# Kernel optimization log

Hardware: AMD Instinct MI355X
Metric: run time of the kernel (lower is better)

The kernel has to match this reference:

```python
import jax, jax.numpy as jnp
import numpy as np

EPS = 1e-15
PROJ_EPS = 1e-5
N_NODES = 100000

def _norm(x):
    return jnp.maximum(jnp.sqrt(jnp.sum(x * x, axis=-1, keepdims=True)), EPS)

def _tanh(x):
    return jnp.tanh(jnp.clip(x, -15.0, 15.0))

def _atanh(x):
    return jnp.arctanh(jnp.clip(x, -1.0 + 1e-7, 1.0 - 1e-7))

def log_map_zero(y):
    n = _norm(y)
    return (_atanh(n) / n) * y

def exp_map_zero(v):
    n = _norm(v)
    return (_tanh(n) / n) * v

def hyperbolic_projection(x):
    # clip norm to 1 - PROJ_EPS (stay inside the Poincare ball)
    n = _norm(x)
    scale = jnp.minimum(jnp.float32(1.0), (1.0 - PROJ_EPS) / n)
    return x * scale

def mobius_addition(x, y):
    x2 = jnp.sum(x * x, axis=-1, keepdims=True)
    y2 = jnp.sum(y * y, axis=-1, keepdims=True)
    xy = jnp.sum(x * y, axis=-1, keepdims=True)
    num = (1.0 + 2.0 * xy + y2) * x + (1.0 - x2) * y
    den = 1.0 + 2.0 * xy + x2 * y2
    return num / jnp.maximum(den, EPS)

def setup_inputs() -> dict:
    key = jax.random.key(0)
    k0, k1, k2, k3, k4, k5 = jax.random.split(key, 6)
    N, E, D_IN, D_OUT = N_NODES, 640000, 128, 128
    # entity embeddings: points inside the Poincare ball
    x = jax.random.normal(k0, (N, D_IN), dtype=jnp.float32) * 0.01
    x = hyperbolic_projection(x)
    # xavier-uniform weight
    a = np.sqrt(6.0 / (D_IN + D_OUT)).astype(np.float32)
    W = jax.random.uniform(k1, (D_IN, D_OUT), minval=-a, maxval=a, dtype=jnp.float32)
    bias = jax.random.normal(k2, (1, D_OUT), dtype=jnp.float32) * 0.01
    adj_row = jax.random.randint(k3, (E,), 0, N, dtype=jnp.int32)
    adj_col = jax.random.randint(k4, (E,), 0, N, dtype=jnp.int32)
    adj_val = jax.random.uniform(k5, (E,), dtype=jnp.float32) * 0.125
    return {"ents_embed_input": x, "W_ent": W, "bias_vec": bias,
            "adj_val": adj_val, "adj_row": adj_row, "adj_col": adj_col}

def reference(ents_embed_input, W_ent, bias_vec, adj_val, adj_row, adj_col):
    # log map to tangent space at origin, then dense linear map
    tangent = log_map_zero(ents_embed_input)                 # [N, D_in]
    mapped = tangent @ W_ent                                 # [N, D_out]
    # sparse adjacency aggregation: out[i] = sum_e val[e] * mapped[col[e]], row[e] == i
    msgs = adj_val[:, None] * mapped[adj_col]                # [E, D_out]
    agg = jax.ops.segment_sum(msgs, adj_row, num_segments=N_NODES)
    h = hyperbolic_projection(exp_map_zero(agg))
    # mobius bias addition
    b = hyperbolic_projection(exp_map_zero(bias_vec))
    out = hyperbolic_projection(mobius_addition(h, b))
    return out
```

## Files before the change

### kernel.cpp

```cpp
#include <hip/hip_runtime.h>
#include <hip/hip_bf16.h>

#define D 128
#define FEPS 1e-15f
#define PROJ_EPS 1e-5f

typedef __attribute__((ext_vector_type(8))) short short8v;
typedef __attribute__((ext_vector_type(4))) float f32x4;

__device__ __forceinline__ unsigned pack_bf16x2(float lo, float hi) {
    __hip_bfloat16 h0 = __float2bfloat16(lo);
    __hip_bfloat16 h1 = __float2bfloat16(hi);
    unsigned u0 = *reinterpret_cast<unsigned short*>(&h0);
    unsigned u1 = *reinterpret_cast<unsigned short*>(&h1);
    return u0 | (u1 << 16);
}

__device__ __forceinline__ float bf_lo(unsigned u) { return __uint_as_float(u << 16); }
__device__ __forceinline__ float bf_hi(unsigned u) { return __uint_as_float(u & 0xffff0000u); }

__device__ __forceinline__ float fast_tanh_clamped(float n) {
    float nc = fminf(n, 15.f);
    float e2 = __expf(2.f * nc);
    return 1.f - __fdividef(2.f, e2 + 1.f);
}

__global__ __launch_bounds__(512) void k_gemm_hist(
    const float* __restrict__ x, const float* __restrict__ W,
    __hip_bfloat16* __restrict__ mapped, int Nn,
    const int* __restrict__ rowi, int* __restrict__ cnt, int E, int GB, int HB)
{
    __shared__ uint4 ls4[2048];

    const int tid = threadIdx.x;

    if (blockIdx.x >= GB) {
        int stride = HB * 512;
        for (int e = (blockIdx.x - GB) * 512 + tid; e < E; e += stride)
            atomicAdd(&cnt[rowi[e]], 1);
        return;
    }

    const int w = tid >> 6, l = tid & 63;
    const int q = l & 15, khi = l >> 4;

#pragma unroll
    for (int it = 0; it < 4; ++it) {
        int i = it * 512 + tid;
        int col = i & 127, kg = i >> 7;
        unsigned p0 = pack_bf16x2(W[(kg * 8 + 0) * D + col], W[(kg * 8 + 1) * D + col]);
        unsigned p1 = pack_bf16x2(W[(kg * 8 + 2) * D + col], W[(kg * 8 + 3) * D + col]);
        unsigned p2 = pack_bf16x2(W[(kg * 8 + 4) * D + col], W[(kg * 8 + 5) * D + col]);
        unsigned p3 = pack_bf16x2(W[(kg * 8 + 6) * D + col], W[(kg * 8 + 7) * D + col]);
        ls4[col * 16 + (kg ^ (col & 15))] = make_uint4(p0, p1, p2, p3);
    }

    const int rowbase = blockIdx.x * 128;
    const int row = rowbase + w * 16 + q;
    const bool rv = row < Nn;
    const float* xr = x + (size_t)row * D;
    float4 xa[8];
    float nn = 0.f;
#pragma unroll
    for (int ks = 0; ks < 4; ++ks) {
        float4 p0 = make_float4(0.f, 0.f, 0.f, 0.f), p1 = p0;
        if (rv) {
            p0 = *reinterpret_cast<const float4*>(xr + ks * 32 + khi * 8);
            p1 = *reinterpret_cast<const float4*>(xr + ks * 32 + khi * 8 + 4);
        }
        xa[2 * ks] = p0; xa[2 * ks + 1] = p1;
        nn += p0.x * p0.x + p0.y * p0.y + p0.z * p0.z + p0.w * p0.w
            + p1.x * p1.x + p1.y * p1.y + p1.z * p1.z + p1.w * p1.w;
    }
    nn += __shfl_xor(nn, 16, 64);
    nn += __shfl_xor(nn, 32, 64);
    float n = fmaxf(sqrtf(nn), FEPS);
    float c = fminf(n, 1.f - 1e-7f);
    float s = __fdividef(0.5f * __logf(__fdividef(1.f + c, 1.f - c)), n);

    union { unsigned u[4]; short8v v; } af[4];
#pragma unroll
    for (int ks = 0; ks < 4; ++ks) {
        float4 p0 = xa[2 * ks], p1 = xa[2 * ks + 1];
        af[ks].u[0] = pack_bf16x2(s * p0.x, s * p0.y);
        af[ks].u[1] = pack_bf16x2(s * p0.z, s * p0.w);
        af[ks].u[2] = pack_bf16x2(s * p1.x, s * p1.y);
        af[ks].u[3] = pack_bf16x2(s * p1.z, s * p1.w);
    }
    __syncthreads();

    f32x4 acc[8];
#pragma unroll
    for (int t = 0; t < 8; ++t) acc[t] = (f32x4){0.f, 0.f, 0.f, 0.f};

    const short8v* lsB = (const short8v*)ls4;
#pragma unroll
    for (int ks = 0; ks < 4; ++ks) {
#pragma unroll
        for (int t = 0; t < 8; ++t) {
            short8v b = lsB[(t * 16 + q) * 16 + ((ks * 4 + khi) ^ q)];
            acc[t] = __builtin_amdgcn_mfma_f32_16x16x32_bf16(af[ks].v, b, acc[t], 0, 0, 0);
        }
    }
    __syncthreads();

    unsigned* lsw = (unsigned*)ls4;
    const int rlbase = w * 16;
#pragma unroll
    for (int t = 0; t < 8; ++t) {
#pragma unroll
        for (int r = 0; r < 4; ++r) {
            float self = acc[t][r];
            float other = __shfl_xor(self, 1, 64);
            unsigned pw = (q & 1) ? pack_bf16x2(other, self) : pack_bf16x2(self, other);
            int rl = rlbase + khi * 4 + r;
            int cp = t * 8 + (q >> 1);
            lsw[rl * 64 + (cp ^ (khi << 3))] = pw;
        }
    }
#pragma unroll
    for (int i4 = 0; i4 < 4; ++i4) {
        int rl = rlbase + i4 * 4 + (l >> 4);
        int ro = rowbase + rl;
        int cp4 = (l & 15) * 4;
        uint4 vv = ls4[(rl * 64 + (cp4 ^ (((rl >> 2) & 3) << 3))) >> 2];
        if (ro < Nn)
            *reinterpret_cast<uint4*>(mapped + (size_t)ro * D + (l & 15) * 8) = vv;
    }
}

__global__ __launch_bounds__(256) void k_scan1(const int* __restrict__ cnt,
                                               int* __restrict__ ex,
                                               int* __restrict__ bsum, int Nn) {
    __shared__ int ts[256];
    int t = threadIdx.x, b = blockIdx.x;
    int base = b * 1024 + t * 4;
    int v0 = (base + 0 < Nn) ? cnt[base + 0] : 0;
    int v1 = (base + 1 < Nn) ? cnt[base + 1] : 0;
    int v2 = (base + 2 < Nn) ? cnt[base + 2] : 0;
    int v3 = (base + 3 < Nn) ? cnt[base + 3] : 0;
    int s = v0 + v1 + v2 + v3;
    ts[t] = s;
    __syncthreads();
    for (int off = 1; off < 256; off <<= 1) {
        int add = (t >= off) ? ts[t - off] : 0;
        __syncthreads();
        ts[t] += add;
        __syncthreads();
    }
    int excl = ts[t] - s;
    if (t == 255) bsum[b] = ts[t];
    if (base + 0 < Nn) ex[base + 0] = excl;
    if (base + 1 < Nn) ex[base + 1] = excl + v0;
    if (base + 2 < Nn) ex[base + 2] = excl + v0 + v1;
    if (base + 3 < Nn) ex[base + 3] = excl + v0 + v1 + v2;
}

__global__ void k_scan2(const int* __restrict__ bsum, int* __restrict__ bsumx, int nb) {
    __shared__ int ts[128];
    int t = threadIdx.x;
    int v = (t < nb) ? bsum[t] : 0;
    ts[t] = v;
    __syncthreads();
    for (int off = 1; off < 128; off <<= 1) {
        int add = (t >= off) ? ts[t - off] : 0;
        __syncthreads();
        ts[t] += add;
        __syncthreads();
    }
    bsumx[t] = ts[t] - v;
}

__global__ __launch_bounds__(256) void k_scan3(int* __restrict__ rowptr,
                                               const int* __restrict__ bsumx,
                                               int* __restrict__ cursor, int Nn, int E) {
    int i = blockIdx.x * 256 + threadIdx.x;
    if (i < Nn) {
        int v = rowptr[i] + bsumx[i >> 10];
        rowptr[i] = v;
        cursor[i] = v;
    }
    if (i == 0) rowptr[Nn] = E;
}

__global__ __launch_bounds__(512) void k_scatter(
    const int* __restrict__ rowi, const int* __restrict__ coli,
    const float* __restrict__ val, int* __restrict__ cursor,
    int2* __restrict__ sedge, int E) {
    int e = blockIdx.x * 512 + threadIdx.x;
    if (e >= E) return;
    int cv = coli[e];
    float vv = val[e];
    int p = atomicAdd(&cursor[rowi[e]], 1);
    sedge[p] = make_int2(cv, __float_as_int(vv));
}

__global__ __launch_bounds__(256) void k_aggfin(
    const uint4* __restrict__ mapped4, const int2* __restrict__ sedge,
    const int* __restrict__ rowptr, const float* __restrict__ bias,
    float* __restrict__ out, int Nn)
{
    const int tid = threadIdx.x;
    const int w = tid >> 6, l = tid & 63;
    const int g = l >> 4, q = l & 15;
    const int row = blockIdx.x * 16 + w * 4 + g;

    float4 rb0 = *reinterpret_cast<const float4*>(bias + q * 8);
    float4 rb1 = *reinterpret_cast<const float4*>(bias + q * 8 + 4);
    float bn2 = rb0.x * rb0.x + rb0.y * rb0.y + rb0.z * rb0.z + rb0.w * rb0.w
              + rb1.x * rb1.x + rb1.y * rb1.y + rb1.z * rb1.z + rb1.w * rb1.w;
#pragma unroll
    for (int o = 8; o > 0; o >>= 1) bn2 += __shfl_xor(bn2, o, 64);
    float bn = fmaxf(sqrtf(bn2), FEPS);
    float bt = fast_tanh_clamped(bn);
    float bs = __fdividef(bt, bn);
    float ben2 = bs * bs * bn2;
    float bpn = fmaxf(sqrtf(ben2), FEPS);
    float bps = fminf(1.f, __fdividef(1.f - PROJ_EPS, bpn));
    float bsc = bs * bps;
    float y2 = bps * bps * ben2;
    float bj[8] = { rb0.x * bsc, rb0.y * bsc, rb0.z * bsc, rb0.w * bsc,
                    rb1.x * bsc, rb1.y * bsc, rb1.z * bsc, rb1.w * bsc };

    if (row >= Nn) return;
    int beg = rowptr[row], end = rowptr[row + 1];

    float acc[8] = {0.f, 0.f, 0.f, 0.f, 0.f, 0.f, 0.f, 0.f};
    int e = beg;
    for (; e + 3 < end; e += 4) {
        int2 d0 = sedge[e], d1 = sedge[e + 1], d2 = sedge[e + 2], d3 = sedge[e + 3];
        uint4 u0 = mapped4[(size_t)d0.x * 16 + q];
        uint4 u1 = mapped4[(size_t)d1.x * 16 + q];
        uint4 u2 = mapped4[(size_t)d2.x * 16 + q];
        uint4 u3 = mapped4[(size_t)d3.x * 16 + q];
        float v0 = __int_as_float(d0.y), v1 = __int_as_float(d1.y);
        float v2 = __int_as_float(d2.y), v3 = __int_as_float(d3.y);
        acc[0] += v0 * bf_lo(u0.x); acc[1] += v0 * bf_hi(u0.x);
        acc[2] += v0 * bf_lo(u0.y); acc[3] += v0 * bf_hi(u0.y);
        acc[4] += v0 * bf_lo(u0.z); acc[5] += v0 * bf_hi(u0.z);
        acc[6] += v0 * bf_lo(u0.w); acc[7] += v0 * bf_hi(u0.w);
        acc[0] += v1 * bf_lo(u1.x); acc[1] += v1 * bf_hi(u1.x);
        acc[2] += v1 * bf_lo(u1.y); acc[3] += v1 * bf_hi(u1.y);
        acc[4] += v1 * bf_lo(u1.z); acc[5] += v1 * bf_hi(u1.z);
        acc[6] += v1 * bf_lo(u1.w); acc[7] += v1 * bf_hi(u1.w);
        acc[0] += v2 * bf_lo(u2.x); acc[1] += v2 * bf_hi(u2.x);
        acc[2] += v2 * bf_lo(u2.y); acc[3] += v2 * bf_hi(u2.y);
        acc[4] += v2 * bf_lo(u2.z); acc[5] += v2 * bf_hi(u2.z);
        acc[6] += v2 * bf_lo(u2.w); acc[7] += v2 * bf_hi(u2.w);
        acc[0] += v3 * bf_lo(u3.x); acc[1] += v3 * bf_hi(u3.x);
        acc[2] += v3 * bf_lo(u3.y); acc[3] += v3 * bf_hi(u3.y);
        acc[4] += v3 * bf_lo(u3.z); acc[5] += v3 * bf_hi(u3.z);
        acc[6] += v3 * bf_lo(u3.w); acc[7] += v3 * bf_hi(u3.w);
    }
    for (; e < end; ++e) {
        int2 d0 = sedge[e];
        uint4 u0 = mapped4[(size_t)d0.x * 16 + q];
        float v0 = __int_as_float(d0.y);
        acc[0] += v0 * bf_lo(u0.x); acc[1] += v0 * bf_hi(u0.x);
        acc[2] += v0 * bf_lo(u0.y); acc[3] += v0 * bf_hi(u0.y);
        acc[4] += v0 * bf_lo(u0.z); acc[5] += v0 * bf_hi(u0.z);
        acc[6] += v0 * bf_lo(u0.w); acc[7] += v0 * bf_hi(u0.w);
    }

    float n2 = 0.f, ab = 0.f;
#pragma unroll
    for (int j = 0; j < 8; ++j) { n2 += acc[j] * acc[j]; ab += acc[j] * bj[j]; }
#pragma unroll
    for (int o = 8; o > 0; o >>= 1) {
        n2 += __shfl_xor(n2, o, 64);
        ab += __shfl_xor(ab, o, 64);
    }

    float n = fmaxf(sqrtf(n2), FEPS);
    float t = fast_tanh_clamped(n);
    float s = __fdividef(t, n);
    float en2 = s * s * n2;
    float pn = fmaxf(sqrtf(en2), FEPS);
    float ps = fminf(1.f, __fdividef(1.f - PROJ_EPS, pn));
    float hs = s * ps;
    float x2 = ps * ps * en2;

    float xy = hs * ab;
    float cA = 1.f + 2.f * xy + y2;
    float cB = 1.f - x2;
    float den = fmaxf(1.f + 2.f * xy + x2 * y2, FEPS);
    float inv = __fdividef(1.f, den);
    float zn2 = inv * inv * (cA * cA * x2 + 2.f * cA * cB * xy + cB * cB * y2);
    float zn = fmaxf(sqrtf(zn2), FEPS);
    float zs = fminf(1.f, __fdividef(1.f - PROJ_EPS, zn));
    float f = inv * zs;
    float chs = cA * hs * f, cBf = cB * f;

    float4 o0 = make_float4(chs * acc[0] + cBf * bj[0], chs * acc[1] + cBf * bj[1],
                            chs * acc[2] + cBf * bj[2], chs * acc[3] + cBf * bj[3]);
    float4 o1 = make_float4(chs * acc[4] + cBf * bj[4], chs * acc[5] + cBf * bj[5],
                            chs * acc[6] + cBf * bj[6], chs * acc[7] + cBf * bj[7]);
    *reinterpret_cast<float4*>(out + (size_t)row * D + q * 8) = o0;
    *reinterpret_cast<float4*>(out + (size_t)row * D + q * 8 + 4) = o1;
}

extern "C" void kernel_launch(void* const* d_in, const int* in_sizes, int n_in,
                              void* d_out, int out_size, void* d_ws, size_t ws_size,
                              hipStream_t stream) {
    const float* x    = (const float*)d_in[0];
    const float* W    = (const float*)d_in[1];
    const float* bias = (const float*)d_in[2];
    const float* val  = (const float*)d_in[3];
    const int*   rowi = (const int*)d_in[4];
    const int*   coli = (const int*)d_in[5];
    const int N = in_sizes[0] / D;
    const int E = in_sizes[3];

    char* ws = (char*)d_ws;
    int*   cnt    = (int*)ws;
    int*   rowptr = (int*)(ws + 400000);
    int*   bsum   = (int*)(ws + 800512);
    int*   bsumx  = (int*)(ws + 801024);
    int*   cursor = (int*)(ws + 801536);
    int2*  sedge  = (int2*)(ws + 1201536);
    __hip_bfloat16* mapped = (__hip_bfloat16*)(ws + 1201536 + (size_t)E * 8);
    float* out = (float*)d_out;

    hipMemsetAsync(cnt, 0, (size_t)N * sizeof(int), stream);

    const int GB = (N + 127) / 128;
    const int HB = 128;
    k_gemm_hist<<<GB + HB, 512, 0, stream>>>(x, W, mapped, N, rowi, cnt, E, GB, HB);

    int nb = (N + 1023) / 1024;
    k_scan1<<<nb, 256, 0, stream>>>(cnt, rowptr, bsum, N);
    k_scan2<<<1, 128, 0, stream>>>(bsum, bsumx, nb);
    k_scan3<<<(N + 255) / 256, 256, 0, stream>>>(rowptr, bsumx, cursor, N, E);

    k_scatter<<<(E + 511) / 512, 512, 0, stream>>>(rowi, coli, val, cursor, sedge, E);
    k_aggfin<<<(N + 15) / 16, 256, 0, stream>>>((const uint4*)mapped, sedge, rowptr,
                                                bias, out, N);
}
```

Measured before the change: 134.1 us.

## Halve gemm block size, use nontemporal edge stores, widen per-lane aggregation width

The GEMM/histogram kernel moves to 256-thread blocks of 64 rows, and the x loads are issued before the W staging so they overlap. The scatter kernel writes packed edge records with nontemporal stores. The aggregation kernel now maps 8 lanes per row with 16 columns each, so a wave covers 8 rows and each lane issues two 16-byte gathers per edge. This aims for more memory-level parallelism per row and less cache pollution, at the cost of more registers per lane and more W staging per block.

```diff
diff --git a/kernel.cpp b/kernel.cpp
--- a/kernel.cpp
+++ b/kernel.cpp
@@ -25,7 +25,18 @@
     return 1.f - __fdividef(2.f, e2 + 1.f);
 }
 
-__global__ __launch_bounds__(512) void k_gemm_hist(
+__device__ __forceinline__ void accum16(float* acc, uint4 a, uint4 b, float v) {
+    acc[0]  += v * bf_lo(a.x); acc[1]  += v * bf_hi(a.x);
+    acc[2]  += v * bf_lo(a.y); acc[3]  += v * bf_hi(a.y);
+    acc[4]  += v * bf_lo(a.z); acc[5]  += v * bf_hi(a.z);
+    acc[6]  += v * bf_lo(a.w); acc[7]  += v * bf_hi(a.w);
+    acc[8]  += v * bf_lo(b.x); acc[9]  += v * bf_hi(b.x);
+    acc[10] += v * bf_lo(b.y); acc[11] += v * bf_hi(b.y);
+    acc[12] += v * bf_lo(b.z); acc[13] += v * bf_hi(b.z);
+    acc[14] += v * bf_lo(b.w); acc[15] += v * bf_hi(b.w);
+}
+
+__global__ __launch_bounds__(256) void k_gemm_hist(
     const float* __restrict__ x, const float* __restrict__ W,
     __hip_bfloat16* __restrict__ mapped, int Nn,
     const int* __restrict__ rowi, int* __restrict__ cnt, int E, int GB, int HB)
@@ -35,8 +46,8 @@
     const int tid = threadIdx.x;
 
     if (blockIdx.x >= GB) {
-        int stride = HB * 512;
-        for (int e = (blockIdx.x - GB) * 512 + tid; e < E; e += stride)
+        int stride = HB * 256;
+        for (int e = (blockIdx.x - GB) * 256 + tid; e < E; e += stride)
             atomicAdd(&cnt[rowi[e]], 1);
         return;
     }
@@ -44,23 +55,11 @@
     const int w = tid >> 6, l = tid & 63;
     const int q = l & 15, khi = l >> 4;
 
-#pragma unroll
-    for (int it = 0; it < 4; ++it) {
-        int i = it * 512 + tid;
-        int col = i & 127, kg = i >> 7;
-        unsigned p0 = pack_bf16x2(W[(kg * 8 + 0) * D + col], W[(kg * 8 + 1) * D + col]);
-        unsigned p1 = pack_bf16x2(W[(kg * 8 + 2) * D + col], W[(kg * 8 + 3) * D + col]);
-        unsigned p2 = pack_bf16x2(W[(kg * 8 + 4) * D + col], W[(kg * 8 + 5) * D + col]);
-        unsigned p3 = pack_bf16x2(W[(kg * 8 + 6) * D + col], W[(kg * 8 + 7) * D + col]);
-        ls4[col * 16 + (kg ^ (col & 15))] = make_uint4(p0, p1, p2, p3);
-    }
-
-    const int rowbase = blockIdx.x * 128;
+    const int rowbase = blockIdx.x * 64;
     const int row = rowbase + w * 16 + q;
     const bool rv = row < Nn;
     const float* xr = x + (size_t)row * D;
     float4 xa[8];
-    float nn = 0.f;
 #pragma unroll
     for (int ks = 0; ks < 4; ++ks) {
         float4 p0 = make_float4(0.f, 0.f, 0.f, 0.f), p1 = p0;
@@ -69,8 +68,24 @@
             p1 = *reinterpret_cast<const float4*>(xr + ks * 32 + khi * 8 + 4);
         }
         xa[2 * ks] = p0; xa[2 * ks + 1] = p1;
-        nn += p0.x * p0.x + p0.y * p0.y + p0.z * p0.z + p0.w * p0.w
-            + p1.x * p1.x + p1.y * p1.y + p1.z * p1.z + p1.w * p1.w;
+    }
+
+#pragma unroll
+    for (int it = 0; it < 8; ++it) {
+        int i = it * 256 + tid;
+        int col = i & 127, kg = i >> 7;
+        unsigned p0 = pack_bf16x2(W[(kg * 8 + 0) * D + col], W[(kg * 8 + 1) * D + col]);
+        unsigned p1 = pack_bf16x2(W[(kg * 8 + 2) * D + col], W[(kg * 8 + 3) * D + col]);
+        unsigned p2 = pack_bf16x2(W[(kg * 8 + 4) * D + col], W[(kg * 8 + 5) * D + col]);
+        unsigned p3 = pack_bf16x2(W[(kg * 8 + 6) * D + col], W[(kg * 8 + 7) * D + col]);
+        ls4[col * 16 + (kg ^ (col & 15))] = make_uint4(p0, p1, p2, p3);
+    }
+
+    float nn = 0.f;
+#pragma unroll
+    for (int j = 0; j < 8; ++j) {
+        float4 p = xa[j];
+        nn += p.x * p.x + p.y * p.y + p.z * p.z + p.w * p.w;
     }
     nn += __shfl_xor(nn, 16, 64);
     nn += __shfl_xor(nn, 32, 64);
@@ -186,13 +201,14 @@
 __global__ __launch_bounds__(512) void k_scatter(
     const int* __restrict__ rowi, const int* __restrict__ coli,
     const float* __restrict__ val, int* __restrict__ cursor,
-    int2* __restrict__ sedge, int E) {
+    long long* __restrict__ sedge, int E) {
     int e = blockIdx.x * 512 + threadIdx.x;
     if (e >= E) return;
     int cv = coli[e];
     float vv = val[e];
     int p = atomicAdd(&cursor[rowi[e]], 1);
-    sedge[p] = make_int2(cv, __float_as_int(vv));
+    long long pkt = ((long long)(unsigned)__float_as_int(vv) << 32) | (unsigned)cv;
+    __builtin_nontemporal_store(pkt, &sedge[p]);
 }
 
 __global__ __launch_bounds__(256) void k_aggfin(
@@ -202,15 +218,20 @@
 {
     const int tid = threadIdx.x;
     const int w = tid >> 6, l = tid & 63;
-    const int g = l >> 4, q = l & 15;
-    const int row = blockIdx.x * 16 + w * 4 + g;
-
-    float4 rb0 = *reinterpret_cast<const float4*>(bias + q * 8);
-    float4 rb1 = *reinterpret_cast<const float4*>(bias + q * 8 + 4);
-    float bn2 = rb0.x * rb0.x + rb0.y * rb0.y + rb0.z * rb0.z + rb0.w * rb0.w
-              + rb1.x * rb1.x + rb1.y * rb1.y + rb1.z * rb1.z + rb1.w * rb1.w;
-#pragma unroll
-    for (int o = 8; o > 0; o >>= 1) bn2 += __shfl_xor(bn2, o, 64);
+    const int g = l >> 3, q = l & 7;
+    const int row = blockIdx.x * 32 + w * 8 + g;
+
+    float bj[16];
+    float bn2 = 0.f;
+#pragma unroll
+    for (int j = 0; j < 4; ++j) {
+        float4 rb = *reinterpret_cast<const float4*>(bias + q * 16 + j * 4);
+        bj[4 * j + 0] = rb.x; bj[4 * j + 1] = rb.y;
+        bj[4 * j + 2] = rb.z; bj[4 * j + 3] = rb.w;
+        bn2 += rb.x * rb.x + rb.y * rb.y + rb.z * rb.z + rb.w * rb.w;
+    }
+#pragma unroll
+    for (int o = 4; o > 0; o >>= 1) bn2 += __shfl_xor(bn2, o, 64);
     float bn = fmaxf(sqrtf(bn2), FEPS);
     float bt = fast_tanh_clamped(bn);
     float bs = __fdividef(bt, bn);
@@ -219,54 +240,40 @@
     float bps = fminf(1.f, __fdividef(1.f - PROJ_EPS, bpn));
     float bsc = bs * bps;
     float y2 = bps * bps * ben2;
-    float bj[8] = { rb0.x * bsc, rb0.y * bsc, rb0.z * bsc, rb0.w * bsc,
-                    rb1.x * bsc, rb1.y * bsc, rb1.z * bsc, rb1.w * bsc };
+#pragma unroll
+    for (int j = 0; j < 16; ++j) bj[j] *= bsc;
 
     if (row >= Nn) return;
     int beg = rowptr[row], end = rowptr[row + 1];
 
-    float acc[8] = {0.f, 0.f, 0.f, 0.f, 0.f, 0.f, 0.f, 0.f};
+    const uint4* mp = mapped4 + 2 * q;
+    float acc[16];
+#pragma unroll
+    for (int j = 0; j < 16; ++j) acc[j] = 0.f;
+
     int e = beg;
     for (; e + 3 < end; e += 4) {
         int2 d0 = sedge[e], d1 = sedge[e + 1], d2 = sedge[e + 2], d3 = sedge[e + 3];
-        uint4 u0 = mapped4[(size_t)d0.x * 16 + q];
-        uint4 u1 = mapped4[(size_t)d1.x * 16 + q];
-        uint4 u2 = mapped4[(size_t)d2.x * 16 + q];
-        uint4 u3 = mapped4[(size_t)d3.x * 16 + q];
-        float v0 = __int_as_float(d0.y), v1 = __int_as_float(d1.y);
-        float v2 = __int_as_float(d2.y), v3 = __int_as_float(d3.y);
-        acc[0] += v0 * bf_lo(u0.x); acc[1] += v0 * bf_hi(u0.x);
-        acc[2] += v0 * bf_lo(u0.y); acc[3] += v0 * bf_hi(u0.y);
-        acc[4] += v0 * bf_lo(u0.z); acc[5] += v0 * bf_hi(u0.z);
-        acc[6] += v0 * bf_lo(u0.w); acc[7] += v0 * bf_hi(u0.w);
-        acc[0] += v1 * bf_lo(u1.x); acc[1] += v1 * bf_hi(u1.x);
-        acc[2] += v1 * bf_lo(u1.y); acc[3] += v1 * bf_hi(u1.y);
-        acc[4] += v1 * bf_lo(u1.z); acc[5] += v1 * bf_hi(u1.z);
-        acc[6] += v1 * bf_lo(u1.w); acc[7] += v1 * bf_hi(u1.w);
-        acc[0] += v2 * bf_lo(u2.x); acc[1] += v2 * bf_hi(u2.x);
-        acc[2] += v2 * bf_lo(u2.y); acc[3] += v2 * bf_hi(u2.y);
-        acc[4] += v2 * bf_lo(u2.z); acc[5] += v2 * bf_hi(u2.z);
-        acc[6] += v2 * bf_lo(u2.w); acc[7] += v2 * bf_hi(u2.w);
-        acc[0] += v3 * bf_lo(u3.x); acc[1] += v3 * bf_hi(u3.x);
-        acc[2] += v3 * bf_lo(u3.y); acc[3] += v3 * bf_hi(u3.y);
-        acc[4] += v3 * bf_lo(u3.z); acc[5] += v3 * bf_hi(u3.z);
-        acc[6] += v3 * bf_lo(u3.w); acc[7] += v3 * bf_hi(u3.w);
+        uint4 a0 = mp[(size_t)d0.x * 16], b0 = mp[(size_t)d0.x * 16 + 1];
+        uint4 a1 = mp[(size_t)d1.x * 16], b1 = mp[(size_t)d1.x * 16 + 1];
+        uint4 a2 = mp[(size_t)d2.x * 16], b2 = mp[(size_t)d2.x * 16 + 1];
+        uint4 a3 = mp[(size_t)d3.x * 16], b3 = mp[(size_t)d3.x * 16 + 1];
+        accum16(acc, a0, b0, __int_as_float(d0.y));
+        accum16(acc, a1, b1, __int_as_float(d1.y));
+        accum16(acc, a2, b2, __int_as_float(d2.y));
+        accum16(acc, a3, b3, __int_as_float(d3.y));
     }
     for (; e < end; ++e) {
-        int2 d0 = sedge[e];
-        uint4 u0 = mapped4[(size_t)d0.x * 16 + q];
-        float v0 = __int_as_float(d0.y);
-        acc[0] += v0 * bf_lo(u0.x); acc[1] += v0 * bf_hi(u0.x);
-        acc[2] += v0 * bf_lo(u0.y); acc[3] += v0 * bf_hi(u0.y);
-        acc[4] += v0 * bf_lo(u0.z); acc[5] += v0 * bf_hi(u0.z);
-        acc[6] += v0 * bf_lo(u0.w); acc[7] += v0 * bf_hi(u0.w);
+        int2 d = sedge[e];
+        uint4 a = mp[(size_t)d.x * 16], b = mp[(size_t)d.x * 16 + 1];
+        accum16(acc, a, b, __int_as_float(d.y));
     }
 
     float n2 = 0.f, ab = 0.f;
 #pragma unroll
-    for (int j = 0; j < 8; ++j) { n2 += acc[j] * acc[j]; ab += acc[j] * bj[j]; }
-#pragma unroll
-    for (int o = 8; o > 0; o >>= 1) {
+    for (int j = 0; j < 16; ++j) { n2 += acc[j] * acc[j]; ab += acc[j] * bj[j]; }
+#pragma unroll
+    for (int o = 4; o > 0; o >>= 1) {
         n2 += __shfl_xor(n2, o, 64);
         ab += __shfl_xor(ab, o, 64);
     }
@@ -291,12 +298,14 @@
     float f = inv * zs;
     float chs = cA * hs * f, cBf = cB * f;
 
-    float4 o0 = make_float4(chs * acc[0] + cBf * bj[0], chs * acc[1] + cBf * bj[1],
-                            chs * acc[2] + cBf * bj[2], chs * acc[3] + cBf * bj[3]);
-    float4 o1 = make_float4(chs * acc[4] + cBf * bj[4], chs * acc[5] + cBf * bj[5],
-                            chs * acc[6] + cBf * bj[6], chs * acc[7] + cBf * bj[7]);
-    *reinterpret_cast<float4*>(out + (size_t)row * D + q * 8) = o0;
-    *reinterpret_cast<float4*>(out + (size_t)row * D + q * 8 + 4) = o1;
+#pragma unroll
+    for (int j = 0; j < 4; ++j) {
+        float4 o4 = make_float4(chs * acc[4 * j + 0] + cBf * bj[4 * j + 0],
+                                chs * acc[4 * j + 1] + cBf * bj[4 * j + 1],
+                                chs * acc[4 * j + 2] + cBf * bj[4 * j + 2],
+                                chs * acc[4 * j + 3] + cBf * bj[4 * j + 3]);
+        *reinterpret_cast<float4*>(out + (size_t)row * D + q * 16 + 4 * j) = o4;
+    }
 }
 
 extern "C" void kernel_launch(void* const* d_in, const int* in_sizes, int n_in,
@@ -317,15 +326,15 @@
     int*   bsum   = (int*)(ws + 800512);
     int*   bsumx  = (int*)(ws + 801024);
     int*   cursor = (int*)(ws + 801536);
-    int2*  sedge  = (int2*)(ws + 1201536);
+    long long* sedge = (long long*)(ws + 1201536);
     __hip_bfloat16* mapped = (__hip_bfloat16*)(ws + 1201536 + (size_t)E * 8);
     float* out = (float*)d_out;
 
     hipMemsetAsync(cnt, 0, (size_t)N * sizeof(int), stream);
 
-    const int GB = (N + 127) / 128;
-    const int HB = 128;
-    k_gemm_hist<<<GB + HB, 512, 0, stream>>>(x, W, mapped, N, rowi, cnt, E, GB, HB);
+    const int GB = (N + 63) / 64;
+    const int HB = 256;
+    k_gemm_hist<<<GB + HB, 256, 0, stream>>>(x, W, mapped, N, rowi, cnt, E, GB, HB);
 
     int nb = (N + 1023) / 1024;
     k_scan1<<<nb, 256, 0, stream>>>(cnt, rowptr, bsum, N);
@@ -333,6 +342,7 @@
     k_scan3<<<(N + 255) / 256, 256, 0, stream>>>(rowptr, bsumx, cursor, N, E);
 
     k_scatter<<<(E + 511) / 512, 512, 0, stream>>>(rowi, coli, val, cursor, sedge, E);
-    k_aggfin<<<(N + 15) / 16, 256, 0, stream>>>((const uint4*)mapped, sedge, rowptr,
+    k_aggfin<<<(N + 31) / 32, 256, 0, stream>>>((const uint4*)mapped,
+                                                (const int2*)sedge, rowptr,
                                                 bias, out, N);
 }
```

Measured after the change: 154.5 us. 15.2% more time.

## Co-schedule GEMM with edge scatter instead of histogram, persistent GEMM blocks

Applied to the files above, without the earlier changes.

Moves the dense bf16 MFMA GEMM out of the histogram kernel and into the scatter kernel, so the GEMM runs concurrently with the atomic edge scatter. The histogram becomes a standalone kernel. GEMM blocks become persistent (384 blocks looping over row tiles) and load W into shared memory once per block, using a separate per-wave LDS staging buffer so the inner loop needs no block barriers. This aims to overlap the compute-heavy GEMM with the longer, latency-bound scatter. In exchange, shared memory use doubles and the grid split is fixed by hand.

```diff
diff --git a/kernel.cpp b/kernel.cpp
--- a/kernel.cpp
+++ b/kernel.cpp
@@ -25,108 +25,10 @@
     return 1.f - __fdividef(2.f, e2 + 1.f);
 }
 
-__global__ __launch_bounds__(512) void k_gemm_hist(
-    const float* __restrict__ x, const float* __restrict__ W,
-    __hip_bfloat16* __restrict__ mapped, int Nn,
-    const int* __restrict__ rowi, int* __restrict__ cnt, int E, int GB, int HB)
-{
-    __shared__ uint4 ls4[2048];
-
-    const int tid = threadIdx.x;
-
-    if (blockIdx.x >= GB) {
-        int stride = HB * 512;
-        for (int e = (blockIdx.x - GB) * 512 + tid; e < E; e += stride)
-            atomicAdd(&cnt[rowi[e]], 1);
-        return;
-    }
-
-    const int w = tid >> 6, l = tid & 63;
-    const int q = l & 15, khi = l >> 4;
-
-#pragma unroll
-    for (int it = 0; it < 4; ++it) {
-        int i = it * 512 + tid;
-        int col = i & 127, kg = i >> 7;
-        unsigned p0 = pack_bf16x2(W[(kg * 8 + 0) * D + col], W[(kg * 8 + 1) * D + col]);
-        unsigned p1 = pack_bf16x2(W[(kg * 8 + 2) * D + col], W[(kg * 8 + 3) * D + col]);
-        unsigned p2 = pack_bf16x2(W[(kg * 8 + 4) * D + col], W[(kg * 8 + 5) * D + col]);
-        unsigned p3 = pack_bf16x2(W[(kg * 8 + 6) * D + col], W[(kg * 8 + 7) * D + col]);
-        ls4[col * 16 + (kg ^ (col & 15))] = make_uint4(p0, p1, p2, p3);
-    }
-
-    const int rowbase = blockIdx.x * 128;
-    const int row = rowbase + w * 16 + q;
-    const bool rv = row < Nn;
-    const float* xr = x + (size_t)row * D;
-    float4 xa[8];
-    float nn = 0.f;
-#pragma unroll
-    for (int ks = 0; ks < 4; ++ks) {
-        float4 p0 = make_float4(0.f, 0.f, 0.f, 0.f), p1 = p0;
-        if (rv) {
-            p0 = *reinterpret_cast<const float4*>(xr + ks * 32 + khi * 8);
-            p1 = *reinterpret_cast<const float4*>(xr + ks * 32 + khi * 8 + 4);
-        }
-        xa[2 * ks] = p0; xa[2 * ks + 1] = p1;
-        nn += p0.x * p0.x + p0.y * p0.y + p0.z * p0.z + p0.w * p0.w
-            + p1.x * p1.x + p1.y * p1.y + p1.z * p1.z + p1.w * p1.w;
-    }
-    nn += __shfl_xor(nn, 16, 64);
-    nn += __shfl_xor(nn, 32, 64);
-    float n = fmaxf(sqrtf(nn), FEPS);
-    float c = fminf(n, 1.f - 1e-7f);
-    float s = __fdividef(0.5f * __logf(__fdividef(1.f + c, 1.f - c)), n);
-
-    union { unsigned u[4]; short8v v; } af[4];
-#pragma unroll
-    for (int ks = 0; ks < 4; ++ks) {
-        float4 p0 = xa[2 * ks], p1 = xa[2 * ks + 1];
-        af[ks].u[0] = pack_bf16x2(s * p0.x, s * p0.y);
-        af[ks].u[1] = pack_bf16x2(s * p0.z, s * p0.w);
-        af[ks].u[2] = pack_bf16x2(s * p1.x, s * p1.y);
-        af[ks].u[3] = pack_bf16x2(s * p1.z, s * p1.w);
-    }
-    __syncthreads();
-
-    f32x4 acc[8];
-#pragma unroll
-    for (int t = 0; t < 8; ++t) acc[t] = (f32x4){0.f, 0.f, 0.f, 0.f};
-
-    const short8v* lsB = (const short8v*)ls4;
-#pragma unroll
-    for (int ks = 0; ks < 4; ++ks) {
-#pragma unroll
-        for (int t = 0; t < 8; ++t) {
-            short8v b = lsB[(t * 16 + q) * 16 + ((ks * 4 + khi) ^ q)];
-            acc[t] = __builtin_amdgcn_mfma_f32_16x16x32_bf16(af[ks].v, b, acc[t], 0, 0, 0);
-        }
-    }
-    __syncthreads();
-
-    unsigned* lsw = (unsigned*)ls4;
-    const int rlbase = w * 16;
-#pragma unroll
-    for (int t = 0; t < 8; ++t) {
-#pragma unroll
-        for (int r = 0; r < 4; ++r) {
-            float self = acc[t][r];
-            float other = __shfl_xor(self, 1, 64);
-            unsigned pw = (q & 1) ? pack_bf16x2(other, self) : pack_bf16x2(self, other);
-            int rl = rlbase + khi * 4 + r;
-            int cp = t * 8 + (q >> 1);
-            lsw[rl * 64 + (cp ^ (khi << 3))] = pw;
-        }
-    }
-#pragma unroll
-    for (int i4 = 0; i4 < 4; ++i4) {
-        int rl = rlbase + i4 * 4 + (l >> 4);
-        int ro = rowbase + rl;
-        int cp4 = (l & 15) * 4;
-        uint4 vv = ls4[(rl * 64 + (cp4 ^ (((rl >> 2) & 3) << 3))) >> 2];
-        if (ro < Nn)
-            *reinterpret_cast<uint4*>(mapped + (size_t)ro * D + (l & 15) * 8) = vv;
-    }
+__global__ __launch_bounds__(512) void k_hist(const int* __restrict__ rowi,
+                                              int* __restrict__ cnt, int E) {
+    int e = blockIdx.x * 512 + threadIdx.x;
+    if (e < E) atomicAdd(&cnt[rowi[e]], 1);
 }
 
 __global__ __launch_bounds__(256) void k_scan1(const int* __restrict__ cnt,
@@ -183,16 +85,118 @@
     if (i == 0) rowptr[Nn] = E;
 }
 
-__global__ __launch_bounds__(512) void k_scatter(
+__global__ __launch_bounds__(512) void k_gemm_scatter(
+    const float* __restrict__ x, const float* __restrict__ W,
+    __hip_bfloat16* __restrict__ mapped, int Nn, int NT, int GBg, int SBs,
     const int* __restrict__ rowi, const int* __restrict__ coli,
     const float* __restrict__ val, int* __restrict__ cursor,
-    int2* __restrict__ sedge, int E) {
-    int e = blockIdx.x * 512 + threadIdx.x;
-    if (e >= E) return;
-    int cv = coli[e];
-    float vv = val[e];
-    int p = atomicAdd(&cursor[rowi[e]], 1);
-    sedge[p] = make_int2(cv, __float_as_int(vv));
+    int2* __restrict__ sedge, int E)
+{
+    __shared__ uint4 lsW4[2048];
+    __shared__ uint4 lsC4[2048];
+
+    const int tid = threadIdx.x;
+
+    if (blockIdx.x >= GBg) {
+        int stride = SBs * 512;
+        for (int e = (blockIdx.x - GBg) * 512 + tid; e < E; e += stride) {
+            int cv = coli[e];
+            float vv = val[e];
+            int p = atomicAdd(&cursor[rowi[e]], 1);
+            sedge[p] = make_int2(cv, __float_as_int(vv));
+        }
+        return;
+    }
+
+    const int w = tid >> 6, l = tid & 63;
+    const int q = l & 15, khi = l >> 4;
+
+#pragma unroll
+    for (int it = 0; it < 4; ++it) {
+        int i = it * 512 + tid;
+        int col = i & 127, kg = i >> 7;
+        unsigned p0 = pack_bf16x2(W[(kg * 8 + 0) * D + col], W[(kg * 8 + 1) * D + col]);
+        unsigned p1 = pack_bf16x2(W[(kg * 8 + 2) * D + col], W[(kg * 8 + 3) * D + col]);
+        unsigned p2 = pack_bf16x2(W[(kg * 8 + 4) * D + col], W[(kg * 8 + 5) * D + col]);
+        unsigned p3 = pack_bf16x2(W[(kg * 8 + 6) * D + col], W[(kg * 8 + 7) * D + col]);
+        lsW4[col * 16 + (kg ^ (col & 15))] = make_uint4(p0, p1, p2, p3);
+    }
+    __syncthreads();
+
+    const short8v* lsB = (const short8v*)lsW4;
+    unsigned* lsc = (unsigned*)lsC4;
+    const int cbase = w * 1024;
+
+#pragma unroll 1
+    for (int tt = blockIdx.x; tt < NT; tt += GBg) {
+        const int rowbase = tt * 128;
+        const int row = rowbase + w * 16 + q;
+        const bool rv = row < Nn;
+        const float* xr = x + (size_t)row * D;
+        float4 xa[8];
+        float nn = 0.f;
+#pragma unroll
+        for (int ks = 0; ks < 4; ++ks) {
+            float4 p0 = make_float4(0.f, 0.f, 0.f, 0.f), p1 = p0;
+            if (rv) {
+                p0 = *reinterpret_cast<const float4*>(xr + ks * 32 + khi * 8);
+                p1 = *reinterpret_cast<const float4*>(xr + ks * 32 + khi * 8 + 4);
+            }
+            xa[2 * ks] = p0; xa[2 * ks + 1] = p1;
+            nn += p0.x * p0.x + p0.y * p0.y + p0.z * p0.z + p0.w * p0.w
+                + p1.x * p1.x + p1.y * p1.y + p1.z * p1.z + p1.w * p1.w;
+        }
+        nn += __shfl_xor(nn, 16, 64);
+        nn += __shfl_xor(nn, 32, 64);
+        float n = fmaxf(sqrtf(nn), FEPS);
+        float c = fminf(n, 1.f - 1e-7f);
+        float s = __fdividef(0.5f * __logf(__fdividef(1.f + c, 1.f - c)), n);
+
+        union { unsigned u[4]; short8v v; } af[4];
+#pragma unroll
+        for (int ks = 0; ks < 4; ++ks) {
+            float4 p0 = xa[2 * ks], p1 = xa[2 * ks + 1];
+            af[ks].u[0] = pack_bf16x2(s * p0.x, s * p0.y);
+            af[ks].u[1] = pack_bf16x2(s * p0.z, s * p0.w);
+            af[ks].u[2] = pack_bf16x2(s * p1.x, s * p1.y);
+            af[ks].u[3] = pack_bf16x2(s * p1.z, s * p1.w);
+        }
+
+        f32x4 acc[8];
+#pragma unroll
+        for (int t = 0; t < 8; ++t) acc[t] = (f32x4){0.f, 0.f, 0.f, 0.f};
+
+#pragma unroll
+        for (int ks = 0; ks < 4; ++ks) {
+#pragma unroll
+            for (int t = 0; t < 8; ++t) {
+                short8v b = lsB[(t * 16 + q) * 16 + ((ks * 4 + khi) ^ q)];
+                acc[t] = __builtin_amdgcn_mfma_f32_16x16x32_bf16(af[ks].v, b, acc[t], 0, 0, 0);
+            }
+        }
+
+#pragma unroll
+        for (int t = 0; t < 8; ++t) {
+#pragma unroll
+            for (int r = 0; r < 4; ++r) {
+                float self = acc[t][r];
+                float other = __shfl_xor(self, 1, 64);
+                unsigned pw = (q & 1) ? pack_bf16x2(other, self) : pack_bf16x2(self, other);
+                int rl = khi * 4 + r;
+                int cp = t * 8 + (q >> 1);
+                lsc[cbase + rl * 64 + (cp ^ (khi << 3))] = pw;
+            }
+        }
+#pragma unroll
+        for (int i4 = 0; i4 < 4; ++i4) {
+            int rl = i4 * 4 + (l >> 4);
+            int ro = rowbase + w * 16 + rl;
+            int cp4 = (l & 15) * 4;
+            uint4 vv = lsC4[(cbase + rl * 64 + (cp4 ^ (i4 << 3))) >> 2];
+            if (ro < Nn)
+                *reinterpret_cast<uint4*>(mapped + (size_t)ro * D + (l & 15) * 8) = vv;
+        }
+    }
 }
 
 __global__ __launch_bounds__(256) void k_aggfin(
@@ -322,17 +326,20 @@
     float* out = (float*)d_out;
 
     hipMemsetAsync(cnt, 0, (size_t)N * sizeof(int), stream);
-
-    const int GB = (N + 127) / 128;
-    const int HB = 128;
-    k_gemm_hist<<<GB + HB, 512, 0, stream>>>(x, W, mapped, N, rowi, cnt, E, GB, HB);
+    k_hist<<<(E + 511) / 512, 512, 0, stream>>>(rowi, cnt, E);
 
     int nb = (N + 1023) / 1024;
     k_scan1<<<nb, 256, 0, stream>>>(cnt, rowptr, bsum, N);
     k_scan2<<<1, 128, 0, stream>>>(bsum, bsumx, nb);
     k_scan3<<<(N + 255) / 256, 256, 0, stream>>>(rowptr, bsumx, cursor, N, E);
 
-    k_scatter<<<(E + 511) / 512, 512, 0, stream>>>(rowi, coli, val, cursor, sedge, E);
-    k_aggfin<<<(N + 15) / 16, 256, 0, stream>>>((const uint4*)mapped, sedge, rowptr,
+    const int NT  = (N + 127) / 128;
+    const int GBg = 384;
+    const int SBs = 128;
+    k_gemm_scatter<<<GBg + SBs, 512, 0, stream>>>(x, W, mapped, N, NT, GBg, SBs,
+                                                  rowi, coli, val, cursor, sedge, E);
+
+    k_aggfin<<<(N + 15) / 16, 256, 0, stream>>>((const uint4*)mapped,
+                                                (const int2*)sedge, rowptr,
                                                 bias, out, N);
 }
```

After: 128.2 us. -4.4%, faster.
